# Performance work log

Measured on AMD Instinct MI355X. Metric: run time of the kernel, lower is better.

## Reference

```python
import jax, jax.numpy as jnp
from jax import lax
import numpy as np

G = 33            # LUT grid size per axis (hard-coded in module)
G3 = G * G * G    # 35937 entries per channel LUT


def _gelu(x):
    return jax.nn.gelu(x, approximate=False)  # torch nn.GELU default = exact erf


def _conv(x, w, b):
    # 3x3 stride-1 padding-1 conv == SAME padding, NCHW/OIHW like torch
    y = lax.conv_general_dilated(x, w, (1, 1), 'SAME',
                                 dimension_numbers=('NCHW', 'OIHW', 'NCHW'))
    return y + b[None, :, None, None]


def _bn(x, g, b, eps=1e-5):
    # eval-mode BatchNorm2d with running_mean=0, running_var=1
    s = g * (1.0 + eps) ** -0.5
    return x * s[None, :, None, None] + b[None, :, None, None]


def _resblock(x, wA, bA, gA, btA, wB, bB, gB, btB):
    h = _gelu(_bn(_conv(x, wA, bA), gA, btA))
    h = _bn(_conv(h, wB, bB), gB, btB)
    return _gelu(h + x)


def _apply_luts(luts_flat, recon):
    # Trilinear 3D-LUT sampling == F.grid_sample(mode='bilinear', padding_mode='border',
    # align_corners=True) on a 5D LUT. grid = recon[...,[2,1,0]]*2-1 means image ch0 (R)
    # indexes LUT dim 2, ch1 (G) dim 3, ch2 (B) dim 4; align_corners maps v->v*(G-1).
    # luts_flat: [B, L*3, G^3] (all num_luts fused into the channel dim, gathered once)
    # recon:     [B, 3, H, W] in [0,1]
    B, C3, _ = luts_flat.shape
    _, _, H, W = recon.shape
    c = jnp.clip(recon * (G - 1.0), 0.0, G - 1.0)      # border clamp
    f0 = jnp.clip(jnp.floor(c), 0.0, G - 2.0)
    t = c - f0                                          # fractional weights [B,3,H,W]
    i0 = f0.astype(jnp.int32)
    r0, g0, b0 = i0[:, 0], i0[:, 1], i0[:, 2]           # [B,H,W] each
    tr, tg, tb = t[:, 0], t[:, 1], t[:, 2]
    out = jnp.zeros((B, C3, H * W), dtype=luts_flat.dtype)
    for dr in (0, 1):
        for dg in (0, 1):
            for db in (0, 1):
                idx = ((r0 + dr) * G + (g0 + dg)) * G + (b0 + db)   # [B,H,W]
                w = ((tr if dr else 1.0 - tr) * (tg if dg else 1.0 - tg)
                     * (tb if db else 1.0 - tb))
                vals = jnp.take_along_axis(luts_flat, idx.reshape(B, 1, H * W), axis=2)
                out = out + vals * w.reshape(B, 1, H * W)
    return out.reshape(B, C3 // 3, 3, H, W)            # [B, L, 3, H, W]


def setup_inputs() -> dict:
    key = jax.random.key(0)
    ks = iter(jax.random.split(key, 32))
    def nrm(shape, s=0.02):
        return jax.random.normal(next(ks), shape, jnp.float32) * s
    B, T, V, E, HID, L, H, W = 4, 1024, 1024, 256, 256, 8, 384, 384
    inp = dict(
        tokens=jax.random.randint(next(ks), (B, T), 0, V),
        img=jax.random.uniform(next(ks), (B, 3, H, W), jnp.float32),
        recon_image=jax.random.uniform(next(ks), (B, 3, H, W), jnp.float32),
        emb_table=nrm((V, E)),
        agg_w1=nrm((E, HID)), agg_b1=jnp.zeros((HID,), jnp.float32),
        agg_w2=nrm((HID, HID)), agg_b2=jnp.zeros((HID,), jnp.float32),
        lut_w1=nrm((HID, HID)), lut_b1=jnp.zeros((HID,), jnp.float32),
        lut_w2=nrm((HID, L * 3 * G3), 0.005),
        lut_b2=jnp.zeros((L * 3 * G3,), jnp.float32),
        wg_w1=nrm((HID, HID // 4)), wg_b1=jnp.zeros((HID // 4,), jnp.float32),
        wg_w2=nrm((HID // 4, L)), wg_b2=jnp.zeros((L,), jnp.float32),
        rp_cin_w=nrm((32, 3, 3, 3)), rp_cin_b=jnp.zeros((32,), jnp.float32),
        rp_rbA_w=nrm((32, 32, 3, 3)), rp_rbA_b=jnp.zeros((32,), jnp.float32),
        rp_rbA_g=jnp.ones((32,), jnp.float32), rp_rbA_bt=jnp.zeros((32,), jnp.float32),
        rp_rbB_w=nrm((32, 32, 3, 3)), rp_rbB_b=jnp.zeros((32,), jnp.float32),
        rp_rbB_g=jnp.ones((32,), jnp.float32), rp_rbB_bt=jnp.zeros((32,), jnp.float32),
        rp_cout_w=nrm((3, 32, 3, 3)), rp_cout_b=jnp.zeros((3,), jnp.float32),
        fu_cin_w=nrm((32, 6, 3, 3)), fu_cin_b=jnp.zeros((32,), jnp.float32),
        fu_rbA_w=nrm((32, 32, 3, 3)), fu_rbA_b=jnp.zeros((32,), jnp.float32),
        fu_rbA_g=jnp.ones((32,), jnp.float32), fu_rbA_bt=jnp.zeros((32,), jnp.float32),
        fu_rbB_w=nrm((32, 32, 3, 3)), fu_rbB_b=jnp.zeros((32,), jnp.float32),
        fu_rbB_g=jnp.ones((32,), jnp.float32), fu_rbB_bt=jnp.zeros((32,), jnp.float32),
        fu_cout_w=nrm((3, 32, 3, 3)), fu_cout_b=jnp.zeros((3,), jnp.float32),
    )
    return inp


def reference(tokens, img, recon_image, emb_table,
              agg_w1, agg_b1, agg_w2, agg_b2,
              lut_w1, lut_b1, lut_w2, lut_b2,
              wg_w1, wg_b1, wg_w2, wg_b2,
              rp_cin_w, rp_cin_b, rp_rbA_w, rp_rbA_b, rp_rbA_g, rp_rbA_bt,
              rp_rbB_w, rp_rbB_b, rp_rbB_g, rp_rbB_bt, rp_cout_w, rp_cout_b,
              fu_cin_w, fu_cin_b, fu_rbA_w, fu_rbA_b, fu_rbA_g, fu_rbA_bt,
              fu_rbB_w, fu_rbB_b, fu_rbB_g, fu_rbB_bt, fu_cout_w, fu_cout_b):
    B = img.shape[0]
    L = wg_w2.shape[1]
    # token features
    emb = emb_table[tokens]                       # [B, T, E]
    tf = jnp.mean(emb, axis=1)                    # [B, E]
    tf = _gelu(tf @ agg_w1 + agg_b1) @ agg_w2 + agg_b2   # [B, HID]
    # dynamic LUTs and fusion weights
    lut_params = _gelu(tf @ lut_w1 + lut_b1) @ lut_w2 + lut_b2   # [B, L*3*G3]
    luts_flat = lut_params.reshape(B, L * 3, G3)
    lw = jax.nn.softmax(_gelu(tf @ wg_w1 + wg_b1) @ wg_w2 + wg_b2, axis=1)  # [B, L]
    # apply all LUTs in one fused gather pass, then weighted sum over LUTs
    lut_out = _apply_luts(luts_flat, recon_image)                # [B, L, 3, H, W]
    fused = jnp.einsum('blchw,bl->bchw', lut_out, lw)            # [B, 3, H, W]
    # residual processing branch on original img
    proc = _gelu(_conv(img, rp_cin_w, rp_cin_b))
    proc = _resblock(proc, rp_rbA_w, rp_rbA_b, rp_rbA_g, rp_rbA_bt,
                     rp_rbB_w, rp_rbB_b, rp_rbB_g, rp_rbB_bt)
    proc = _conv(proc, rp_cout_w, rp_cout_b)
    # fusion
    comb = jnp.concatenate([fused, proc], axis=1)                # [B, 6, H, W]
    out = _gelu(_conv(comb, fu_cin_w, fu_cin_b))
    out = _resblock(out, fu_rbA_w, fu_rbA_b, fu_rbA_g, fu_rbA_bt,
                    fu_rbB_w, fu_rbB_b, fu_rbB_g, fu_rbB_bt)
    out = _conv(out, fu_cout_w, fu_cout_b)
    return out + img
```

## Files before the change

### kernel.cpp

```cpp
#include <hip/hip_runtime.h>
#include <hip/hip_bf16.h>
#include <math.h>

#define BB    4
#define TT    1024
#define EE    256
#define HIDD  256
#define LLUT  8
#define HGT   384
#define WID   384
#define HWPX  147456
#define GSZ   33
#define G3    35937
#define NCOL  862488

typedef __attribute__((ext_vector_type(8))) short bf16x8;
typedef __attribute__((ext_vector_type(4))) float f32x4;

__device__ __forceinline__ float gelu_f(float x) {
    float s = 1.5957691216057308f * x * (1.0f + 0.044715f * x * x);
    float e = __expf(s);
    return x - x / (e + 1.0f);
}

__device__ __forceinline__ ushort f2bf(float x) {
    uint u = __float_as_uint(x);
    return (ushort)((u + 0x7FFFu + ((u >> 16) & 1u)) >> 16);
}
__device__ __forceinline__ uint pack2bf(float a, float b) {
    return (uint)f2bf(a) | ((uint)f2bf(b) << 16);
}
__device__ __forceinline__ float bf2f_lo(uint u) { return __uint_as_float(u << 16); }
__device__ __forceinline__ float bf2f_hi(uint u) { return __uint_as_float(u & 0xFFFF0000u); }

#define TH2 8
#define TW2 64
#define NTX (WID / TW2)
#define NTY (HGT / TH2)
#define NBLK (NTX * NTY * BB)
#define CHUNK (NBLK / 8)
#define HALO_H2 10
#define HALO_W2 66
#define CSTR 40

__global__ __launch_bounds__(256) void pack_wconv_kernel(
    const float* __restrict__ w0, const float* __restrict__ w1,
    const float* __restrict__ w2, const float* __restrict__ w3,
    const float* __restrict__ c0w, const float* __restrict__ c1w,
    const float* __restrict__ w6, ushort* __restrict__ wpk)
{
    const int layer = blockIdx.x;
    if (layer < 6) {
        const float* w = (layer == 0) ? w0 : (layer == 1) ? w1 :
                         (layer == 2) ? w2 : (layer == 3) ? w3 :
                         (layer == 4) ? c0w : c1w;
        const bool small = (layer >= 4);
        ushort* dst = wpk + layer * 9216;
        for (int i = threadIdx.x; i < 9216; i += 256) {
            const int j    = i & 7;
            const int lane = (i >> 3) & 63;
            const int half = (i >> 9) & 1;
            const int tap  = i >> 10;
            const int co = half * 16 + (lane & 15);
            const int ci = (lane >> 4) * 8 + j;
            float v = 0.f;
            if (!small || co < 3) v = w[co * 288 + ci * 9 + tap];
            dst[i] = f2bf(v);
        }
    } else {
        ushort* dst = wpk + 6 * 9216;
        for (int i = threadIdx.x; i < 2048; i += 256) {
            const int j    = i & 7;
            const int lane = (i >> 3) & 63;
            const int half = (i >> 9) & 1;
            const int ks   = i >> 10;
            const int co = half * 16 + (lane & 15);
            const int k  = ks * 32 + (lane >> 4) * 8 + j;
            float v = 0.f;
            if (k < 54) { const int tap = k / 6, ci = k - 6 * tap;
                          v = w6[co * 54 + ci * 9 + tap]; }
            dst[i] = f2bf(v);
        }
    }
}

__global__ __launch_bounds__(256) void emb_partial_kernel(
    const int* __restrict__ tokens, const float* __restrict__ emb,
    float* __restrict__ partial)
{
    const int s = blockIdx.x, b = blockIdx.y, tid = threadIdx.x;
    const int* tok = tokens + b * TT + s * 16;
    float acc = 0.f;
#pragma unroll
    for (int t = 0; t < 16; ++t) acc += emb[tok[t] * EE + tid];
    partial[(b * 64 + s) * EE + tid] = acc;
}

__global__ __launch_bounds__(1024) void mlp_head_kernel(
    const float* __restrict__ partial,
    const float* __restrict__ aw1, const float* __restrict__ ab1,
    const float* __restrict__ aw2, const float* __restrict__ ab2,
    const float* __restrict__ lw1, const float* __restrict__ lb1,
    const float* __restrict__ gw1, const float* __restrict__ gb1,
    const float* __restrict__ gw2, const float* __restrict__ gb2,
    float* __restrict__ h3_out, float* __restrict__ lw_out)
{
    const int b = blockIdx.x;
    const int tid = threadIdx.x;
    const int o = tid & 255;
    const int q = tid >> 8;
    __shared__ float tf[256], h1[256], tf2s[256], h4[64], lg[8];
    __shared__ float red[4][256];

    {
        float acc = 0.f;
#pragma unroll
        for (int s = 0; s < 16; ++s)
            acc += partial[(b * 64 + q * 16 + s) * EE + o];
        red[q][o] = acc;
    }
    __syncthreads();
    if (tid < 256)
        tf[tid] = (red[0][tid] + red[1][tid] + red[2][tid] + red[3][tid]) * (1.0f / TT);
    __syncthreads();

    {
        float s = 0.f;
#pragma unroll 8
        for (int j = 0; j < 64; ++j) {
            const int k = (q << 6) + j;
            s += tf[k] * aw1[k * HIDD + o];
        }
        red[q][o] = s;
    }
    __syncthreads();
    if (tid < 256)
        h1[tid] = gelu_f(red[0][tid] + red[1][tid] + red[2][tid] + red[3][tid] + ab1[tid]);
    __syncthreads();

    {
        float s = 0.f;
#pragma unroll 8
        for (int j = 0; j < 64; ++j) {
            const int k = (q << 6) + j;
            s += h1[k] * aw2[k * HIDD + o];
        }
        red[q][o] = s;
    }
    __syncthreads();
    if (tid < 256)
        tf2s[tid] = red[0][tid] + red[1][tid] + red[2][tid] + red[3][tid] + ab2[tid];
    __syncthreads();

    {
        float s = 0.f;
#pragma unroll 8
        for (int j = 0; j < 64; ++j) {
            const int k = (q << 6) + j;
            s += tf2s[k] * lw1[k * HIDD + o];
        }
        red[q][o] = s;
    }
    __syncthreads();
    if (tid < 256)
        h3_out[b * HIDD + tid] =
            gelu_f(red[0][tid] + red[1][tid] + red[2][tid] + red[3][tid] + lb1[tid]);
    __syncthreads();

    {
        const int o64 = tid & 63, q16 = tid >> 6;
        float s = 0.f;
#pragma unroll
        for (int j = 0; j < 16; ++j) {
            const int k = q16 * 16 + j;
            s += tf2s[k] * gw1[k * 64 + o64];
        }
        ((float*)red)[q16 * 64 + o64] = s;
    }
    __syncthreads();
    if (tid < 64) {
        float s = gb1[tid];
#pragma unroll
        for (int r = 0; r < 16; ++r) s += ((float*)red)[r * 64 + tid];
        h4[tid] = gelu_f(s);
    }
    __syncthreads();

    if (tid < 8) {
        float s = gb2[tid];
#pragma unroll 8
        for (int k = 0; k < 64; ++k) s += h4[k] * gw2[k * LLUT + tid];
        lg[tid] = s;
    }
    __syncthreads();
    if (tid == 0) {
        float m = lg[0];
        for (int i = 1; i < LLUT; ++i) m = fmaxf(m, lg[i]);
        float ssum = 0.f, ex[LLUT];
        for (int i = 0; i < LLUT; ++i) { ex[i] = expf(lg[i] - m); ssum += ex[i]; }
        for (int i = 0; i < LLUT; ++i) lw_out[b * LLUT + i] = ex[i] / ssum;
    }
}

__global__ __launch_bounds__(256) void lut_fused_kernel(
    const float* __restrict__ h3, const float* __restrict__ lwv,
    const float* __restrict__ w2, const float* __restrict__ b2,
    float* __restrict__ clut)
{
    __shared__ float h[BB * HIDD];
    __shared__ float lws[BB * LLUT];
    const int tid = threadIdx.x;
    for (int i = tid; i < BB * HIDD; i += 256) h[i] = h3[i];
    if (tid < BB * LLUT) lws[tid] = lwv[tid];
    __syncthreads();

    const int idx = blockIdx.x * 256 + tid;
    if (idx >= 3 * G3) return;
    const int c = idx / G3, v = idx - c * G3;

    float acc[BB][LLUT];
#pragma unroll
    for (int b = 0; b < BB; ++b)
#pragma unroll
        for (int l = 0; l < LLUT; ++l) acc[b][l] = 0.f;

    const float* wbase = w2 + (long)c * G3 + v;
#pragma unroll 4
    for (int k = 0; k < HIDD; ++k) {
        const float* row = wbase + (long)k * NCOL;
        float wl[LLUT];
#pragma unroll
        for (int l = 0; l < LLUT; ++l) wl[l] = row[l * 3 * G3];
#pragma unroll
        for (int b = 0; b < BB; ++b) {
            const float hb = h[b * HIDD + k];
#pragma unroll
            for (int l = 0; l < LLUT; ++l) acc[b][l] += wl[l] * hb;
        }
    }

    float bb[LLUT];
#pragma unroll
    for (int l = 0; l < LLUT; ++l) bb[l] = b2[(long)(l * 3 + c) * G3 + v];

#pragma unroll
    for (int b = 0; b < BB; ++b) {
        float s = 0.f;
#pragma unroll
        for (int l = 0; l < LLUT; ++l) s += lws[b * LLUT + l] * (acc[b][l] + bb[l]);
        clut[(long)(b * 3 + c) * G3 + v] = s;
    }
}

__global__ __launch_bounds__(256) void applylut_kernel(
    const float* __restrict__ clut, const float* __restrict__ recon,
    ushort* __restrict__ comb)
{
    const int p = blockIdx.x * 256 + threadIdx.x;
    const int b = blockIdx.y;

    const float* rc = recon + (long)b * 3 * HWPX;
    float cr = fminf(fmaxf(rc[p] * 32.f, 0.f), 32.f);
    float cg = fminf(fmaxf(rc[HWPX + p] * 32.f, 0.f), 32.f);
    float cb = fminf(fmaxf(rc[2 * HWPX + p] * 32.f, 0.f), 32.f);
    float fr = fminf(floorf(cr), 31.f);
    float fg = fminf(floorf(cg), 31.f);
    float fb = fminf(floorf(cb), 31.f);
    float tr = cr - fr, tg = cg - fg, tb_ = cb - fb;
    int idx = (((int)fr * GSZ + (int)fg) * GSZ + (int)fb);
    float c[3];
#pragma unroll
    for (int ch = 0; ch < 3; ++ch) {
        const float* lut = clut + (long)(b * 3 + ch) * G3;
        float v000 = lut[idx],                  v001 = lut[idx + 1];
        float v010 = lut[idx + GSZ],            v011 = lut[idx + GSZ + 1];
        float v100 = lut[idx + GSZ * GSZ],      v101 = lut[idx + GSZ * GSZ + 1];
        float v110 = lut[idx + GSZ * GSZ + GSZ], v111 = lut[idx + GSZ * GSZ + GSZ + 1];
        float c00 = v000 + (v001 - v000) * tb_;
        float c01 = v010 + (v011 - v010) * tb_;
        float c10 = v100 + (v101 - v100) * tb_;
        float c11 = v110 + (v111 - v110) * tb_;
        float c0 = c00 + (c01 - c00) * tg;
        float c1 = c10 + (c11 - c10) * tg;
        c[ch] = c0 + (c1 - c0) * tr;
    }
    uint2 u;
    u.x = pack2bf(c[0], c[1]);
    u.y = pack2bf(c[2], 0.f);
    *(uint2*)(comb + ((long)b * HWPX + p) * 8) = u;
}

__global__ __launch_bounds__(256) void conv_in3_kernel(
    const float* __restrict__ img, const float* __restrict__ wgt,
    const float* __restrict__ bias, ushort* __restrict__ out)
{
    const int tid = threadIdx.x;
    const int p0 = (blockIdx.x * 256 + tid) * 2;
    const int b = blockIdx.y;
    const int hh = p0 / WID, ww = p0 - hh * WID;

    float acc[32][2];
#pragma unroll
    for (int o = 0; o < 32; ++o) { float bv = bias[o]; acc[o][0] = bv; acc[o][1] = bv; }

    const bool wlo = (ww > 0), whi = (ww + 2 < WID);
#pragma unroll
    for (int ci = 0; ci < 3; ++ci) {
        const float* ip = img + (long)(b * 3 + ci) * HWPX;
        float x[3][4];
#pragma unroll
        for (int dh = 0; dh < 3; ++dh) {
            const int hs = hh + dh - 1;
            const bool hok = (hs >= 0) && (hs < HGT);
            const float* rp_ = ip + hs * WID + ww;
            x[dh][0] = (hok && wlo) ? rp_[-1] : 0.f;
            x[dh][1] = hok ? rp_[0] : 0.f;
            x[dh][2] = hok ? rp_[1] : 0.f;
            x[dh][3] = (hok && whi) ? rp_[2] : 0.f;
        }
#pragma unroll
        for (int o = 0; o < 32; ++o) {
            const float* wv = wgt + o * 27 + ci * 9;
#pragma unroll
            for (int dh = 0; dh < 3; ++dh)
#pragma unroll
                for (int dw = 0; dw < 3; ++dw) {
                    const float w = wv[dh * 3 + dw];
                    acc[o][0] += x[dh][dw]     * w;
                    acc[o][1] += x[dh][dw + 1] * w;
                }
        }
    }

    ushort* op = out + ((long)b * HWPX + p0) * 32;
#pragma unroll
    for (int px = 0; px < 2; ++px) {
        uint u[16];
#pragma unroll
        for (int o2 = 0; o2 < 16; ++o2)
            u[o2] = pack2bf(gelu_f(acc[2 * o2][px]), gelu_f(acc[2 * o2 + 1][px]));
        uint4* dst = (uint4*)(op + px * 32);
#pragma unroll
        for (int q = 0; q < 4; ++q)
            dst[q] = make_uint4(u[4 * q], u[4 * q + 1], u[4 * q + 2], u[4 * q + 3]);
    }
}

template <bool HAS_RES>
__global__ __launch_bounds__(512, 6) void conv32_mfma(
    const ushort* __restrict__ in, const ushort* __restrict__ res,
    const ushort* __restrict__ wpk, const float* __restrict__ bias,
    const float* __restrict__ bn_g, const float* __restrict__ bn_bt,
    ushort* __restrict__ out)
{
    __shared__ ushort halo[HALO_H2 * HALO_W2 * CSTR];
    __shared__ float s_scale[32], s_shift[32];

    const int tid = threadIdx.x;
    const int bid = blockIdx.x;
    const int t   = (bid & 7) * CHUNK + (bid >> 3);
    const int tx  = t % NTX;
    const int rem = t / NTX;
    const int ty  = rem % NTY;
    const int b   = rem / NTY;
    const int h0 = ty * TH2;
    const int w0 = tx * TW2;

    if (tid < 32) {
        float sg = bn_g[tid] * 0.9999950000375f;
        s_scale[tid] = sg;
        s_shift[tid] = bias[tid] * sg + bn_bt[tid];
    }

    const ushort* inb = in + (long)b * HWPX * 32;
    for (int i = tid; i < HALO_H2 * HALO_W2 * 4; i += 512) {
        const int row = i / (HALO_W2 * 4);
        const int rem2 = i - row * (HALO_W2 * 4);
        const int px = rem2 >> 2, q = rem2 & 3;
        const int gh = h0 + row - 1, gw = w0 + px - 1;
        uint4 v = make_uint4(0u, 0u, 0u, 0u);
        if (gh >= 0 && gh < HGT && gw >= 0 && gw < WID)
            v = *(const uint4*)(inb + ((long)gh * WID + gw) * 32 + q * 8);
        *(uint4*)(&halo[(row * HALO_W2 + px) * CSTR + q * 8]) = v;
    }
    __syncthreads();

    const int lane = tid & 63, wid = tid >> 6;
    const int l15 = lane & 15, kg = lane >> 4;
    const int r = wid;
    const ushort* wlane = wpk + lane * 8;

    f32x4 acc[4][2];
#pragma unroll
    for (int f = 0; f < 4; ++f)
#pragma unroll
        for (int cf = 0; cf < 2; ++cf)
            acc[f][cf] = (f32x4){0.f, 0.f, 0.f, 0.f};

#pragma unroll
    for (int tap = 0; tap < 9; ++tap) {
        const int dh = tap / 3, dw = tap - dh * 3;
        const bf16x8 a0 = *(const bf16x8*)(wlane + (tap * 2 + 0) * 512);
        const bf16x8 a1 = *(const bf16x8*)(wlane + (tap * 2 + 1) * 512);
#pragma unroll
        for (int f = 0; f < 4; ++f) {
            const int c0 = f * 16;
            const bf16x8 bfv = *(const bf16x8*)(
                &halo[((r + dh) * HALO_W2 + (c0 + dw + l15)) * CSTR + kg * 8]);
            acc[f][0] = __builtin_amdgcn_mfma_f32_16x16x32_bf16(a0, bfv, acc[f][0], 0, 0, 0);
            acc[f][1] = __builtin_amdgcn_mfma_f32_16x16x32_bf16(a1, bfv, acc[f][1], 0, 0, 0);
        }
    }

#pragma unroll
    for (int f = 0; f < 4; ++f) {
        const int c0 = f * 16;
        const long gpx = (long)b * HWPX + (long)(h0 + r) * WID + (w0 + c0 + l15);
#pragma unroll
        for (int cf = 0; cf < 2; ++cf) {
            const int co0 = cf * 16 + kg * 4;
            const float4 sc = *(const float4*)(&s_scale[co0]);
            const float4 sh = *(const float4*)(&s_shift[co0]);
            float v0 = acc[f][cf][0] * sc.x + sh.x;
            float v1 = acc[f][cf][1] * sc.y + sh.y;
            float v2 = acc[f][cf][2] * sc.z + sh.z;
            float v3 = acc[f][cf][3] * sc.w + sh.w;
            if (HAS_RES) {
                const uint2 rv = *(const uint2*)(res + gpx * 32 + co0);
                v0 += bf2f_lo(rv.x); v1 += bf2f_hi(rv.x);
                v2 += bf2f_lo(rv.y); v3 += bf2f_hi(rv.y);
            }
            uint2 o;
            o.x = pack2bf(gelu_f(v0), gelu_f(v1));
            o.y = pack2bf(gelu_f(v2), gelu_f(v3));
            *(uint2*)(out + gpx * 32 + co0) = o;
        }
    }
}

template <bool FINAL>
__global__ __launch_bounds__(512, 4) void conv_out3_mfma(
    const ushort* __restrict__ in, const ushort* __restrict__ wpk,
    const float* __restrict__ bias, const float* __restrict__ img,
    float* __restrict__ outp, ushort* __restrict__ comb)
{
    __shared__ ushort halo[HALO_H2 * HALO_W2 * CSTR];

    const int tid = threadIdx.x;
    const int bid = blockIdx.x;
    const int t   = (bid & 7) * CHUNK + (bid >> 3);
    const int tx  = t % NTX;
    const int rem = t / NTX;
    const int ty  = rem % NTY;
    const int b   = rem / NTY;
    const int h0 = ty * TH2;
    const int w0 = tx * TW2;

    const ushort* inb = in + (long)b * HWPX * 32;
    for (int i = tid; i < HALO_H2 * HALO_W2 * 4; i += 512) {
        const int row = i / (HALO_W2 * 4);
        const int rem2 = i - row * (HALO_W2 * 4);
        const int px = rem2 >> 2, q = rem2 & 3;
        const int gh = h0 + row - 1, gw = w0 + px - 1;
        uint4 v = make_uint4(0u, 0u, 0u, 0u);
        if (gh >= 0 && gh < HGT && gw >= 0 && gw < WID)
            v = *(const uint4*)(inb + ((long)gh * WID + gw) * 32 + q * 8);
        *(uint4*)(&halo[(row * HALO_W2 + px) * CSTR + q * 8]) = v;
    }
    __syncthreads();

    const int lane = tid & 63, wid = tid >> 6;
    const int l15 = lane & 15, kg = lane >> 4;
    const int r = wid;
    const ushort* wlane = wpk + lane * 8;

    f32x4 acc[4];
#pragma unroll
    for (int f = 0; f < 4; ++f) acc[f] = (f32x4){0.f, 0.f, 0.f, 0.f};

#pragma unroll
    for (int tap = 0; tap < 9; ++tap) {
        const int dh = tap / 3, dw = tap - dh * 3;
        const bf16x8 a0 = *(const bf16x8*)(wlane + (tap * 2 + 0) * 512);
#pragma unroll
        for (int f = 0; f < 4; ++f) {
            const int c0 = f * 16;
            const bf16x8 bfv = *(const bf16x8*)(
                &halo[((r + dh) * HALO_W2 + (c0 + dw + l15)) * CSTR + kg * 8]);
            acc[f] = __builtin_amdgcn_mfma_f32_16x16x32_bf16(a0, bfv, acc[f], 0, 0, 0);
        }
    }

    if (kg == 0) {
        const float b0 = bias[0], b1 = bias[1], b2v = bias[2];
#pragma unroll
        for (int f = 0; f < 4; ++f) {
            const int p = (h0 + r) * WID + (w0 + f * 16 + l15);
            const long gpx = (long)b * HWPX + p;
            float v0 = acc[f][0] + b0;
            float v1 = acc[f][1] + b1;
            float v2 = acc[f][2] + b2v;
            if (FINAL) {
                outp[(long)(b * 3 + 0) * HWPX + p] = v0 + img[(long)(b * 3 + 0) * HWPX + p];
                outp[(long)(b * 3 + 1) * HWPX + p] = v1 + img[(long)(b * 3 + 1) * HWPX + p];
                outp[(long)(b * 3 + 2) * HWPX + p] = v2 + img[(long)(b * 3 + 2) * HWPX + p];
            } else {
                uint2 u;
                u.x = pack2bf(v0, v1);
                u.y = pack2bf(v2, 0.f);
                *(uint2*)(comb + gpx * 8 + 4) = u;
            }
        }
    }
}

__global__ __launch_bounds__(512) void conv_in6_mfma(
    const ushort* __restrict__ comb, const ushort* __restrict__ wpk6,
    const float* __restrict__ bias, ushort* __restrict__ out)
{
    __shared__ ushort chalo[HALO_H2 * HALO_W2 * 8];
    __shared__ float s_bias[32];

    const int tid = threadIdx.x;
    const int bid = blockIdx.x;
    const int t   = (bid & 7) * CHUNK + (bid >> 3);
    const int tx  = t % NTX;
    const int rem = t / NTX;
    const int ty  = rem % NTY;
    const int b   = rem / NTY;
    const int h0 = ty * TH2;
    const int w0 = tx * TW2;

    if (tid < 32) s_bias[tid] = bias[tid];

    const ushort* cb = comb + (long)b * HWPX * 8;
    for (int i = tid; i < HALO_H2 * HALO_W2; i += 512) {
        const int row = i / HALO_W2, px = i - row * HALO_W2;
        const int gh = h0 + row - 1, gw = w0 + px - 1;
        uint4 v = make_uint4(0u, 0u, 0u, 0u);
        if (gh >= 0 && gh < HGT && gw >= 0 && gw < WID)
            v = *(const uint4*)(cb + ((long)gh * WID + gw) * 8);
        *(uint4*)(&chalo[i * 8]) = v;
    }
    __syncthreads();

    const int lane = tid & 63, wid = tid >> 6;
    const int l15 = lane & 15, kg = lane >> 4;
    const int r = wid;
    const ushort* wl6 = wpk6 + lane * 8;

    f32x4 acc[4][2];
#pragma unroll
    for (int f = 0; f < 4; ++f)
#pragma unroll
        for (int cf = 0; cf < 2; ++cf)
            acc[f][cf] = (f32x4){0.f, 0.f, 0.f, 0.f};

#pragma unroll
    for (int ks = 0; ks < 2; ++ks) {
        const bf16x8 a0 = *(const bf16x8*)(wl6 + (ks * 2 + 0) * 512);
        const bf16x8 a1 = *(const bf16x8*)(wl6 + (ks * 2 + 1) * 512);
#pragma unroll
        for (int f = 0; f < 4; ++f) {
            const int c0 = f * 16;
            bf16x8 bv;
#pragma unroll
            for (int j = 0; j < 8; ++j) {
                const int k = ks * 32 + kg * 8 + j;
                ushort val = 0;
                if (k < 54) {
                    const int tap = k / 6, ci = k - 6 * tap;
                    const int dh = tap / 3, dwp = tap - 3 * dh;
                    const int slot = ci + (ci >= 3 ? 1 : 0);
                    val = chalo[((r + dh) * HALO_W2 + (c0 + dwp + l15)) * 8 + slot];
                }
                bv[j] = (short)val;
            }
            acc[f][0] = __builtin_amdgcn_mfma_f32_16x16x32_bf16(a0, bv, acc[f][0], 0, 0, 0);
            acc[f][1] = __builtin_amdgcn_mfma_f32_16x16x32_bf16(a1, bv, acc[f][1], 0, 0, 0);
        }
    }

#pragma unroll
    for (int f = 0; f < 4; ++f) {
        const int c0 = f * 16;
        const long gpx = (long)b * HWPX + (long)(h0 + r) * WID + (w0 + c0 + l15);
#pragma unroll
        for (int cf = 0; cf < 2; ++cf) {
            const int co0 = cf * 16 + kg * 4;
            const float4 bv4 = *(const float4*)(&s_bias[co0]);
            float v0 = acc[f][cf][0] + bv4.x;
            float v1 = acc[f][cf][1] + bv4.y;
            float v2 = acc[f][cf][2] + bv4.z;
            float v3 = acc[f][cf][3] + bv4.w;
            uint2 o;
            o.x = pack2bf(gelu_f(v0), gelu_f(v1));
            o.y = pack2bf(gelu_f(v2), gelu_f(v3));
            *(uint2*)(out + gpx * 32 + co0) = o;
        }
    }
}

extern "C" void kernel_launch(void* const* d_in, const int* in_sizes, int n_in,
                              void* d_out, int out_size, void* d_ws, size_t ws_size,
                              hipStream_t stream)
{
    const int*   tokens  = (const int*)d_in[0];
    const float* img     = (const float*)d_in[1];
    const float* recon   = (const float*)d_in[2];
    const float* emb     = (const float*)d_in[3];
    const float* agg_w1  = (const float*)d_in[4];
    const float* agg_b1  = (const float*)d_in[5];
    const float* agg_w2  = (const float*)d_in[6];
    const float* agg_b2  = (const float*)d_in[7];
    const float* lut_w1  = (const float*)d_in[8];
    const float* lut_b1  = (const float*)d_in[9];
    const float* lut_w2  = (const float*)d_in[10];
    const float* lut_b2  = (const float*)d_in[11];
    const float* wg_w1   = (const float*)d_in[12];
    const float* wg_b1   = (const float*)d_in[13];
    const float* wg_w2   = (const float*)d_in[14];
    const float* wg_b2   = (const float*)d_in[15];
    const float* rp_cin_w = (const float*)d_in[16];
    const float* rp_cin_b = (const float*)d_in[17];
    const float* rp_rbA_w = (const float*)d_in[18];
    const float* rp_rbA_b = (const float*)d_in[19];
    const float* rp_rbA_g = (const float*)d_in[20];
    const float* rp_rbA_bt= (const float*)d_in[21];
    const float* rp_rbB_w = (const float*)d_in[22];
    const float* rp_rbB_b = (const float*)d_in[23];
    const float* rp_rbB_g = (const float*)d_in[24];
    const float* rp_rbB_bt= (const float*)d_in[25];
    const float* rp_cout_w= (const float*)d_in[26];
    const float* rp_cout_b= (const float*)d_in[27];
    const float* fu_cin_w = (const float*)d_in[28];
    const float* fu_cin_b = (const float*)d_in[29];
    const float* fu_rbA_w = (const float*)d_in[30];
    const float* fu_rbA_b = (const float*)d_in[31];
    const float* fu_rbA_g = (const float*)d_in[32];
    const float* fu_rbA_bt= (const float*)d_in[33];
    const float* fu_rbB_w = (const float*)d_in[34];
    const float* fu_rbB_b = (const float*)d_in[35];
    const float* fu_rbB_g = (const float*)d_in[36];
    const float* fu_rbB_bt= (const float*)d_in[37];
    const float* fu_cout_w= (const float*)d_in[38];
    const float* fu_cout_b= (const float*)d_in[39];

    float* ws = (float*)d_ws;
    float*  h3      = ws;
    float*  lwv     = ws + 1024;
    float*  partial = ws + 2048;
    float*  clut    = ws + 69632;
    ushort* wpack   = (ushort*)(ws + 524288);
    ushort* comb    = (ushort*)(ws + 589824);
    ushort* act0    = (ushort*)(ws + 3145728);
    ushort* act1    = (ushort*)(ws + 12582912);
    ushort* act2    = (ushort*)(ws + 22020096);
    float*  outp    = (float*)d_out;

    pack_wconv_kernel<<<dim3(7), dim3(256), 0, stream>>>(
        rp_rbA_w, rp_rbB_w, fu_rbA_w, fu_rbB_w, rp_cout_w, fu_cout_w,
        fu_cin_w, wpack);

    emb_partial_kernel<<<dim3(64, BB), dim3(256), 0, stream>>>(tokens, emb, partial);
    mlp_head_kernel<<<dim3(BB), dim3(1024), 0, stream>>>(
        partial, agg_w1, agg_b1, agg_w2, agg_b2,
        lut_w1, lut_b1, wg_w1, wg_b1, wg_w2, wg_b2, h3, lwv);

    lut_fused_kernel<<<dim3((3 * G3 + 255) / 256), dim3(256), 0, stream>>>(
        h3, lwv, lut_w2, lut_b2, clut);

    const dim3 g1(HWPX / 256, BB), g2(HWPX / 512, BB), blk(256);
    const dim3 gm(NBLK), bm(512);

    conv_in3_kernel<<<g2, blk, 0, stream>>>(img, rp_cin_w, rp_cin_b, act0);
    conv32_mfma<false><<<gm, bm, 0, stream>>>(
        act0, nullptr, wpack + 0 * 9216, rp_rbA_b, rp_rbA_g, rp_rbA_bt, act1);
    conv32_mfma<true><<<gm, bm, 0, stream>>>(
        act1, act0, wpack + 1 * 9216, rp_rbB_b, rp_rbB_g, rp_rbB_bt, act2);

    applylut_kernel<<<g1, blk, 0, stream>>>(clut, recon, comb);
    conv_out3_mfma<false><<<gm, bm, 0, stream>>>(
        act2, wpack + 4 * 9216, rp_cout_b, nullptr, nullptr, comb);

    conv_in6_mfma<<<gm, bm, 0, stream>>>(comb, wpack + 6 * 9216, fu_cin_b, act0);
    conv32_mfma<false><<<gm, bm, 0, stream>>>(
        act0, nullptr, wpack + 2 * 9216, fu_rbA_b, fu_rbA_g, fu_rbA_bt, act1);
    conv32_mfma<true><<<gm, bm, 0, stream>>>(
        act1, act0, wpack + 3 * 9216, fu_rbB_b, fu_rbB_g, fu_rbB_bt, act2);
    conv_out3_mfma<true><<<gm, bm, 0, stream>>>(
        act2, wpack + 5 * 9216, fu_cout_b, img, outp, nullptr);
}
```

Baseline: 508.4 us.

## Port 3-channel input conv to MFMA and fuse LUT apply into output conv

Replaces the scalar FP32 3->32 input convolution with an MFMA kernel. The new kernel stages a bf16 image halo in shared memory and packs the 27-element K dimension into a single 16x16x32 MFMA per output fragment, using a new packed weight slot. It also removes the standalone trilinear LUT kernel and runs that work inside the residual-branch conv_out3 kernel, writing the LUT channels of the combined buffer there. This saves one launch and one pass over the recon data, at the cost of bf16 rounding on the input convolution and extra work in the conv_out3 tail.

```diff
diff --git a/kernel.cpp b/kernel.cpp
--- a/kernel.cpp
+++ b/kernel.cpp
@@ -43,11 +43,15 @@
 #define HALO_W2 66
 #define CSTR 40
 
+#define WPK_IN6 55296
+#define WPK_IN3 57344
+
 __global__ __launch_bounds__(256) void pack_wconv_kernel(
     const float* __restrict__ w0, const float* __restrict__ w1,
     const float* __restrict__ w2, const float* __restrict__ w3,
     const float* __restrict__ c0w, const float* __restrict__ c1w,
-    const float* __restrict__ w6, ushort* __restrict__ wpk)
+    const float* __restrict__ w6, const float* __restrict__ w7,
+    ushort* __restrict__ wpk)
 {
     const int layer = blockIdx.x;
     if (layer < 6) {
@@ -67,8 +71,8 @@
             if (!small || co < 3) v = w[co * 288 + ci * 9 + tap];
             dst[i] = f2bf(v);
         }
-    } else {
-        ushort* dst = wpk + 6 * 9216;
+    } else if (layer == 6) {
+        ushort* dst = wpk + WPK_IN6;
         for (int i = threadIdx.x; i < 2048; i += 256) {
             const int j    = i & 7;
             const int lane = (i >> 3) & 63;
@@ -81,6 +85,19 @@
                           v = w6[co * 54 + ci * 9 + tap]; }
             dst[i] = f2bf(v);
         }
+    } else {
+        ushort* dst = wpk + WPK_IN3;
+        for (int i = threadIdx.x; i < 1024; i += 256) {
+            const int j    = i & 7;
+            const int lane = (i >> 3) & 63;
+            const int half = (i >> 9) & 1;
+            const int co = half * 16 + (lane & 15);
+            const int k  = (lane >> 4) * 8 + j;
+            float v = 0.f;
+            if (k < 27) { const int tap = k / 3, ci = k - 3 * tap;
+                          v = w7[co * 27 + ci * 9 + tap]; }
+            dst[i] = f2bf(v);
+        }
     }
 }
 
@@ -252,97 +269,86 @@
     }
 }
 
-__global__ __launch_bounds__(256) void applylut_kernel(
-    const float* __restrict__ clut, const float* __restrict__ recon,
-    ushort* __restrict__ comb)
-{
-    const int p = blockIdx.x * 256 + threadIdx.x;
-    const int b = blockIdx.y;
-
-    const float* rc = recon + (long)b * 3 * HWPX;
-    float cr = fminf(fmaxf(rc[p] * 32.f, 0.f), 32.f);
-    float cg = fminf(fmaxf(rc[HWPX + p] * 32.f, 0.f), 32.f);
-    float cb = fminf(fmaxf(rc[2 * HWPX + p] * 32.f, 0.f), 32.f);
-    float fr = fminf(floorf(cr), 31.f);
-    float fg = fminf(floorf(cg), 31.f);
-    float fb = fminf(floorf(cb), 31.f);
-    float tr = cr - fr, tg = cg - fg, tb_ = cb - fb;
-    int idx = (((int)fr * GSZ + (int)fg) * GSZ + (int)fb);
-    float c[3];
-#pragma unroll
-    for (int ch = 0; ch < 3; ++ch) {
-        const float* lut = clut + (long)(b * 3 + ch) * G3;
-        float v000 = lut[idx],                  v001 = lut[idx + 1];
-        float v010 = lut[idx + GSZ],            v011 = lut[idx + GSZ + 1];
-        float v100 = lut[idx + GSZ * GSZ],      v101 = lut[idx + GSZ * GSZ + 1];
-        float v110 = lut[idx + GSZ * GSZ + GSZ], v111 = lut[idx + GSZ * GSZ + GSZ + 1];
-        float c00 = v000 + (v001 - v000) * tb_;
-        float c01 = v010 + (v011 - v010) * tb_;
-        float c10 = v100 + (v101 - v100) * tb_;
-        float c11 = v110 + (v111 - v110) * tb_;
-        float c0 = c00 + (c01 - c00) * tg;
-        float c1 = c10 + (c11 - c10) * tg;
-        c[ch] = c0 + (c1 - c0) * tr;
-    }
-    uint2 u;
-    u.x = pack2bf(c[0], c[1]);
-    u.y = pack2bf(c[2], 0.f);
-    *(uint2*)(comb + ((long)b * HWPX + p) * 8) = u;
-}
-
-__global__ __launch_bounds__(256) void conv_in3_kernel(
-    const float* __restrict__ img, const float* __restrict__ wgt,
+__global__ __launch_bounds__(512) void conv_in3_mfma(
+    const float* __restrict__ img, const ushort* __restrict__ wpk3,
     const float* __restrict__ bias, ushort* __restrict__ out)
 {
+    __shared__ ushort ihalo[HALO_H2 * HALO_W2 * 4];
+    __shared__ float s_bias[32];
+
     const int tid = threadIdx.x;
-    const int p0 = (blockIdx.x * 256 + tid) * 2;
-    const int b = blockIdx.y;
-    const int hh = p0 / WID, ww = p0 - hh * WID;
-
-    float acc[32][2];
-#pragma unroll
-    for (int o = 0; o < 32; ++o) { float bv = bias[o]; acc[o][0] = bv; acc[o][1] = bv; }
-
-    const bool wlo = (ww > 0), whi = (ww + 2 < WID);
-#pragma unroll
-    for (int ci = 0; ci < 3; ++ci) {
-        const float* ip = img + (long)(b * 3 + ci) * HWPX;
-        float x[3][4];
-#pragma unroll
-        for (int dh = 0; dh < 3; ++dh) {
-            const int hs = hh + dh - 1;
-            const bool hok = (hs >= 0) && (hs < HGT);
-            const float* rp_ = ip + hs * WID + ww;
-            x[dh][0] = (hok && wlo) ? rp_[-1] : 0.f;
-            x[dh][1] = hok ? rp_[0] : 0.f;
-            x[dh][2] = hok ? rp_[1] : 0.f;
-            x[dh][3] = (hok && whi) ? rp_[2] : 0.f;
-        }
-#pragma unroll
-        for (int o = 0; o < 32; ++o) {
-            const float* wv = wgt + o * 27 + ci * 9;
-#pragma unroll
-            for (int dh = 0; dh < 3; ++dh)
-#pragma unroll
-                for (int dw = 0; dw < 3; ++dw) {
-                    const float w = wv[dh * 3 + dw];
-                    acc[o][0] += x[dh][dw]     * w;
-                    acc[o][1] += x[dh][dw + 1] * w;
-                }
-        }
-    }
-
-    ushort* op = out + ((long)b * HWPX + p0) * 32;
-#pragma unroll
-    for (int px = 0; px < 2; ++px) {
-        uint u[16];
-#pragma unroll
-        for (int o2 = 0; o2 < 16; ++o2)
-            u[o2] = pack2bf(gelu_f(acc[2 * o2][px]), gelu_f(acc[2 * o2 + 1][px]));
-        uint4* dst = (uint4*)(op + px * 32);
-#pragma unroll
-        for (int q = 0; q < 4; ++q)
-            dst[q] = make_uint4(u[4 * q], u[4 * q + 1], u[4 * q + 2], u[4 * q + 3]);
+    const int bid = blockIdx.x;
+    const int t   = (bid & 7) * CHUNK + (bid >> 3);
+    const int tx  = t % NTX;
+    const int rem = t / NTX;
+    const int ty  = rem % NTY;
+    const int b   = rem / NTY;
+    const int h0 = ty * TH2;
+    const int w0 = tx * TW2;
+
+    if (tid < 32) s_bias[tid] = bias[tid];
+
+    const float* imb = img + (long)b * 3 * HWPX;
+    for (int i = tid; i < HALO_H2 * HALO_W2; i += 512) {
+        const int row = i / HALO_W2, px = i - row * HALO_W2;
+        const int gh = h0 + row - 1, gw = w0 + px - 1;
+        float c0v = 0.f, c1v = 0.f, c2v = 0.f;
+        if (gh >= 0 && gh < HGT && gw >= 0 && gw < WID) {
+            const int p = gh * WID + gw;
+            c0v = imb[p]; c1v = imb[HWPX + p]; c2v = imb[2 * HWPX + p];
+        }
+        uint2 u; u.x = pack2bf(c0v, c1v); u.y = pack2bf(c2v, 0.f);
+        *(uint2*)(&ihalo[i * 4]) = u;
+    }
+    __syncthreads();
+
+    const int lane = tid & 63, wid = tid >> 6;
+    const int l15 = lane & 15, kg = lane >> 4;
+    const int r = wid;
+    const ushort* wl3 = wpk3 + lane * 8;
+
+    const bf16x8 a0 = *(const bf16x8*)(wl3 + 0 * 512);
+    const bf16x8 a1 = *(const bf16x8*)(wl3 + 1 * 512);
+
+    f32x4 acc[4][2];
+#pragma unroll
+    for (int f = 0; f < 4; ++f)
+#pragma unroll
+        for (int cf = 0; cf < 2; ++cf)
+            acc[f][cf] = (f32x4){0.f, 0.f, 0.f, 0.f};
+
+#pragma unroll
+    for (int f = 0; f < 4; ++f) {
+        const int c0 = f * 16;
+        bf16x8 bv;
+#pragma unroll
+        for (int j = 0; j < 8; ++j) {
+            const int k = kg * 8 + j;
+            ushort val = 0;
+            if (k < 27) {
+                const int tap = k / 3, ci = k - 3 * tap;
+                const int dh = tap / 3, dwp = tap - 3 * dh;
+                val = ihalo[((r + dh) * HALO_W2 + (c0 + dwp + l15)) * 4 + ci];
+            }
+            bv[j] = (short)val;
+        }
+        acc[f][0] = __builtin_amdgcn_mfma_f32_16x16x32_bf16(a0, bv, acc[f][0], 0, 0, 0);
+        acc[f][1] = __builtin_amdgcn_mfma_f32_16x16x32_bf16(a1, bv, acc[f][1], 0, 0, 0);
+    }
+
+#pragma unroll
+    for (int f = 0; f < 4; ++f) {
+        const int c0 = f * 16;
+        const long gpx = (long)b * HWPX + (long)(h0 + r) * WID + (w0 + c0 + l15);
+#pragma unroll
+        for (int cf = 0; cf < 2; ++cf) {
+            const int co0 = cf * 16 + kg * 4;
+            const float4 bv4 = *(const float4*)(&s_bias[co0]);
+            uint2 o;
+            o.x = pack2bf(gelu_f(acc[f][cf][0] + bv4.x), gelu_f(acc[f][cf][1] + bv4.y));
+            o.y = pack2bf(gelu_f(acc[f][cf][2] + bv4.z), gelu_f(acc[f][cf][3] + bv4.w));
+            *(uint2*)(out + gpx * 32 + co0) = o;
+        }
     }
 }
 
@@ -442,7 +448,8 @@
 __global__ __launch_bounds__(512, 4) void conv_out3_mfma(
     const ushort* __restrict__ in, const ushort* __restrict__ wpk,
     const float* __restrict__ bias, const float* __restrict__ img,
-    float* __restrict__ outp, ushort* __restrict__ comb)
+    float* __restrict__ outp, ushort* __restrict__ comb,
+    const float* __restrict__ clut, const float* __restrict__ recon)
 {
     __shared__ ushort halo[HALO_H2 * HALO_W2 * CSTR];
 
@@ -512,6 +519,40 @@
             }
         }
     }
+
+    if (!FINAL) {
+        const int row = tid >> 6, col = tid & 63;
+        const int p = (h0 + row) * WID + (w0 + col);
+        const float* rc = recon + (long)b * 3 * HWPX;
+        float cr = fminf(fmaxf(rc[p] * 32.f, 0.f), 32.f);
+        float cg = fminf(fmaxf(rc[HWPX + p] * 32.f, 0.f), 32.f);
+        float cb = fminf(fmaxf(rc[2 * HWPX + p] * 32.f, 0.f), 32.f);
+        float fr = fminf(floorf(cr), 31.f);
+        float fg = fminf(floorf(cg), 31.f);
+        float fb = fminf(floorf(cb), 31.f);
+        float tr = cr - fr, tg = cg - fg, tb_ = cb - fb;
+        int idx = (((int)fr * GSZ + (int)fg) * GSZ + (int)fb);
+        float c[3];
+#pragma unroll
+        for (int ch = 0; ch < 3; ++ch) {
+            const float* lut = clut + (long)(b * 3 + ch) * G3;
+            float v000 = lut[idx],                  v001 = lut[idx + 1];
+            float v010 = lut[idx + GSZ],            v011 = lut[idx + GSZ + 1];
+            float v100 = lut[idx + GSZ * GSZ],      v101 = lut[idx + GSZ * GSZ + 1];
+            float v110 = lut[idx + GSZ * GSZ + GSZ], v111 = lut[idx + GSZ * GSZ + GSZ + 1];
+            float c00 = v000 + (v001 - v000) * tb_;
+            float c01 = v010 + (v011 - v010) * tb_;
+            float c10 = v100 + (v101 - v100) * tb_;
+            float c11 = v110 + (v111 - v110) * tb_;
+            float c0 = c00 + (c01 - c00) * tg;
+            float c1 = c10 + (c11 - c10) * tg;
+            c[ch] = c0 + (c1 - c0) * tr;
+        }
+        uint2 u;
+        u.x = pack2bf(c[0], c[1]);
+        u.y = pack2bf(c[2], 0.f);
+        *(uint2*)(comb + ((long)b * HWPX + p) * 8) = u;
+    }
 }
 
 __global__ __launch_bounds__(512) void conv_in6_mfma(
@@ -589,13 +630,9 @@
         for (int cf = 0; cf < 2; ++cf) {
             const int co0 = cf * 16 + kg * 4;
             const float4 bv4 = *(const float4*)(&s_bias[co0]);
-            float v0 = acc[f][cf][0] + bv4.x;
-            float v1 = acc[f][cf][1] + bv4.y;
-            float v2 = acc[f][cf][2] + bv4.z;
-            float v3 = acc[f][cf][3] + bv4.w;
             uint2 o;
-            o.x = pack2bf(gelu_f(v0), gelu_f(v1));
-            o.y = pack2bf(gelu_f(v2), gelu_f(v3));
+            o.x = pack2bf(gelu_f(acc[f][cf][0] + bv4.x), gelu_f(acc[f][cf][1] + bv4.y));
+            o.y = pack2bf(gelu_f(acc[f][cf][2] + bv4.z), gelu_f(acc[f][cf][3] + bv4.w));
             *(uint2*)(out + gpx * 32 + co0) = o;
         }
     }
@@ -658,9 +695,9 @@
     ushort* act2    = (ushort*)(ws + 22020096);
     float*  outp    = (float*)d_out;
 
-    pack_wconv_kernel<<<dim3(7), dim3(256), 0, stream>>>(
+    pack_wconv_kernel<<<dim3(8), dim3(256), 0, stream>>>(
         rp_rbA_w, rp_rbB_w, fu_rbA_w, fu_rbB_w, rp_cout_w, fu_cout_w,
-        fu_cin_w, wpack);
+        fu_cin_w, rp_cin_w, wpack);
 
     emb_partial_kernel<<<dim3(64, BB), dim3(256), 0, stream>>>(tokens, emb, partial);
     mlp_head_kernel<<<dim3(BB), dim3(1024), 0, stream>>>(
@@ -670,24 +707,22 @@
     lut_fused_kernel<<<dim3((3 * G3 + 255) / 256), dim3(256), 0, stream>>>(
         h3, lwv, lut_w2, lut_b2, clut);
 
-    const dim3 g1(HWPX / 256, BB), g2(HWPX / 512, BB), blk(256);
     const dim3 gm(NBLK), bm(512);
 
-    conv_in3_kernel<<<g2, blk, 0, stream>>>(img, rp_cin_w, rp_cin_b, act0);
+    conv_in3_mfma<<<gm, bm, 0, stream>>>(img, wpack + WPK_IN3, rp_cin_b, act0);
     conv32_mfma<false><<<gm, bm, 0, stream>>>(
         act0, nullptr, wpack + 0 * 9216, rp_rbA_b, rp_rbA_g, rp_rbA_bt, act1);
     conv32_mfma<true><<<gm, bm, 0, stream>>>(
         act1, act0, wpack + 1 * 9216, rp_rbB_b, rp_rbB_g, rp_rbB_bt, act2);
 
-    applylut_kernel<<<g1, blk, 0, stream>>>(clut, recon, comb);
     conv_out3_mfma<false><<<gm, bm, 0, stream>>>(
-        act2, wpack + 4 * 9216, rp_cout_b, nullptr, nullptr, comb);
-
-    conv_in6_mfma<<<gm, bm, 0, stream>>>(comb, wpack + 6 * 9216, fu_cin_b, act0);
+        act2, wpack + 4 * 9216, rp_cout_b, nullptr, nullptr, comb, clut, recon);
+
+    conv_in6_mfma<<<gm, bm, 0, stream>>>(comb, wpack + WPK_IN6, fu_cin_b, act0);
     conv32_mfma<false><<<gm, bm, 0, stream>>>(
         act0, nullptr, wpack + 2 * 9216, fu_rbA_b, fu_rbA_g, fu_rbA_bt, act1);
     conv32_mfma<true><<<gm, bm, 0, stream>>>(
         act1, act0, wpack + 3 * 9216, fu_rbB_b, fu_rbB_g, fu_rbB_bt, act2);
     conv_out3_mfma<true><<<gm, bm, 0, stream>>>(
-        act2, wpack + 5 * 9216, fu_cout_b, img, outp, nullptr);
-}
+        act2, wpack + 5 * 9216, fu_cout_b, img, outp, nullptr, nullptr, nullptr);
+}
```

Result: faster. 476.4 us (-6.3%).
